# Performance work log

Hardware: AMD Instinct MI355X
Metric: run time of the kernel (lower is better)

The kernel has to match this reference:

```python
import jax, jax.numpy as jnp
import numpy as np

BETA = 0.25


def setup_inputs() -> dict:
    key = jax.random.key(0)
    k1, k2 = jax.random.split(key)
    latents = jax.random.normal(k1, (16, 4096, 256), dtype=jnp.float32)
    K = 1024
    # torch init: uniform(-1/K, 1/K)
    codebook = jax.random.uniform(k2, (K, 256), dtype=jnp.float32, minval=-1.0 / K, maxval=1.0 / K)
    return {"latents": latents, "codebook": codebook}


def reference(latents, codebook):
    D = codebook.shape[1]
    flat = latents.reshape(-1, D)  # [N, D]
    dist = (jnp.sum(flat * flat, axis=1, keepdims=True)
            + jnp.sum(codebook * codebook, axis=1)
            - 2.0 * jnp.matmul(flat, codebook.T))
    encoding_inds = jnp.argmin(dist, axis=1)  # [N]
    # gather nearest codebook vectors (equivalent to one-hot @ codebook)
    quantized = codebook[encoding_inds].reshape(latents.shape)
    commitment_loss = jnp.mean((jax.lax.stop_gradient(quantized) - latents) ** 2)
    embedding_loss = jnp.mean((quantized - jax.lax.stop_gradient(latents)) ** 2)
    vq_loss = commitment_loss * BETA + embedding_loss
    # straight-through estimator
    quantized_st = latents + jax.lax.stop_gradient(quantized - latents)
    return quantized_st, vq_loss
```

## Files before the change

kernel.cpp:

```cpp
#include <hip/hip_runtime.h>

typedef __attribute__((ext_vector_type(4))) float f32x4;
typedef __attribute__((ext_vector_type(2))) long i64x2;

#define SCALE 262144.0f
#define NEG2S -524288.0f
#define INV_S2 1.4551915228366852e-11f

static __device__ __forceinline__ unsigned umin2(unsigned a, unsigned b) { return a < b ? a : b; }

static __device__ __forceinline__ float dec_e4m3(unsigned b) {
  int e = (b >> 3) & 15, m = b & 7;
  float v = e ? ldexpf((float)(8 + m), e - 10) : ldexpf((float)m, -9);
  return (b & 0x80) ? -v : v;
}

__global__ void vq_prep(const float* __restrict__ cb,
                        float* __restrict__ norms,
                        unsigned char* __restrict__ cbh,
                        float* __restrict__ loss_out) {
  if (blockIdx.x == 0 && threadIdx.x == 0) *loss_out = 0.0f;
  const int lane = threadIdx.x & 63;
  const int code = (blockIdx.x * blockDim.x + threadIdx.x) >> 6;
  const f32x4 v = ((const f32x4*)(cb + (long)code * 256))[lane];
  unsigned w = __builtin_amdgcn_cvt_pk_fp8_f32(v[0] * SCALE, v[1] * SCALE, 0, false);
  w = __builtin_amdgcn_cvt_pk_fp8_f32(v[2] * SCALE, v[3] * SCALE, w, true);
  float n = 0.f;
#pragma unroll
  for (int j = 0; j < 4; ++j) {
    float d = dec_e4m3((w >> (8 * j)) & 0xFFu);
    n = __builtin_fmaf(d, d, n);
  }
  const int newpos = ((lane >> 1) & 3) * 64 + (lane >> 3) * 8 + (lane & 1) * 4;
  *(unsigned*)(cbh + (long)code * 256 + newpos) = w;
#pragma unroll
  for (int m = 1; m < 64; m <<= 1) n += __shfl_xor(n, m);
  if (lane == 0) norms[code] = n;
}

#define NTHR 512
#define RPB 256
#define NTILE 16

__global__ __launch_bounds__(NTHR, 2)
void vq_main(const float* __restrict__ X,
             const float* __restrict__ CB,
             const float* __restrict__ norms_g,
             const unsigned char* __restrict__ cbh,
             float* __restrict__ out,
             float* __restrict__ loss_out,
             float lscale) {
  __shared__ __attribute__((aligned(16))) unsigned char Xs[2][4096];
  __shared__ unsigned mgAll[NTILE][8][16];
  __shared__ unsigned idxArr[RPB];
  __shared__ float wsumX[8], wsumS[8];

  const int t = threadIdx.x;
  const int lane = t & 63;
  const int wave = t >> 6;
  const int lo16 = lane & 15;
  const int hi = lane >> 4;
  const long rowBase = (long)blockIdx.x * RPB;

  long b[8][8];
  float nrm[8];
  {
    const char* cbB = (const char*)cbh;
#pragma unroll
    for (int n = 0; n < 8; ++n) {
      const int code = wave * 128 + n * 16 + lo16;
      const char* src = cbB + (long)code * 256 + hi * 64;
#pragma unroll
      for (int kp = 0; kp < 4; ++kp) {
        i64x2 bb = *(const i64x2*)(src + kp * 16);
        b[n][2 * kp] = bb.x;
        b[n][2 * kp + 1] = bb.y;
      }
      nrm[n] = norms_g[code];
    }
  }

  const int srow = t >> 5;
  const int sch = t & 31;
  const unsigned sdst =
      (unsigned)(srow * 256 + ((((sch & 3) * 64) + ((sch >> 2) * 8)) ^ ((srow & 7) << 3)));
  const f32x4* xv = (const f32x4*)(X + (rowBase + srow) * 256) + sch * 2;

  float xn = 0.f;
  f32x4 p0, p1;

#define CVT_WRITE(BUF)                                                                    \
  {                                                                                       \
    float s0 = 0.f;                                                                       \
    _Pragma("unroll") for (int j = 0; j < 4; ++j) s0 = __builtin_fmaf(p0[j], p0[j], s0);  \
    _Pragma("unroll") for (int j = 0; j < 4; ++j) s0 = __builtin_fmaf(p1[j], p1[j], s0);  \
    xn += s0;                                                                             \
    unsigned w0 = __builtin_amdgcn_cvt_pk_fp8_f32(p0[0], p0[1], 0, false);                \
    w0 = __builtin_amdgcn_cvt_pk_fp8_f32(p0[2], p0[3], w0, true);                         \
    unsigned w1 = __builtin_amdgcn_cvt_pk_fp8_f32(p1[0], p1[1], 0, false);                \
    w1 = __builtin_amdgcn_cvt_pk_fp8_f32(p1[2], p1[3], w1, true);                         \
    *(long*)((char*)&Xs[BUF][0] + sdst) = (long)(unsigned)w0 | ((long)w1 << 32);          \
  }

  p0 = __builtin_nontemporal_load(xv);
  p1 = __builtin_nontemporal_load(xv + 1);
  CVT_WRITE(0);
  p0 = __builtin_nontemporal_load(xv + 1024);
  p1 = __builtin_nontemporal_load(xv + 1024 + 1);
  __syncthreads();

  for (int tt = 0; tt < NTILE; ++tt) {
    const char* xb = (const char*)&Xs[tt & 1][0];
    const unsigned abase = (unsigned)(lo16 * 256 + hi * 64);
    const unsigned aswz = (unsigned)((lo16 & 7) << 3);
    long a[8];
#pragma unroll
    for (int ks = 0; ks < 8; ++ks)
      a[ks] = *(const long*)(xb + ((abase + ks * 8) ^ aswz));

    f32x4 acc[8];
#pragma unroll
    for (int n = 0; n < 8; ++n) {
      f32x4 z = {0.f, 0.f, 0.f, 0.f};
      acc[n] = z;
    }
    __builtin_amdgcn_s_setprio(1);
#pragma unroll
    for (int ks = 0; ks < 8; ++ks)
#pragma unroll
      for (int n = 0; n < 8; ++n)
        acc[n] = __builtin_amdgcn_mfma_f32_16x16x32_fp8_fp8(a[ks], b[n][ks], acc[n], 0, 0, 0);
    __builtin_amdgcn_s_setprio(0);

    unsigned bst[4] = {0xFFFFFFFFu, 0xFFFFFFFFu, 0xFFFFFFFFu, 0xFFFFFFFFu};
#pragma unroll
    for (int n = 0; n < 8; ++n) {
      const float nf = nrm[n];
      const unsigned code = (unsigned)(wave * 128 + n * 16 + lo16);
#pragma unroll
      for (int r = 0; r < 4; ++r) {
        float sv = __builtin_fmaf(NEG2S, acc[n][r], nf);
        unsigned u = __float_as_uint(sv);
        u = ((int)u < 0) ? ~u : (u | 0x80000000u);
        bst[r] = umin2(bst[r], (u & 0xFFFFFC00u) | code);
      }
    }
#pragma unroll
    for (int r = 0; r < 4; ++r) {
#pragma unroll
      for (int msk = 1; msk < 16; msk <<= 1)
        bst[r] = umin2(bst[r], (unsigned)__shfl_xor((int)bst[r], msk));
    }
    if (lo16 == 0) {
#pragma unroll
      for (int r = 0; r < 4; ++r) mgAll[tt][wave][hi * 4 + r] = bst[r];
    }

    if (tt + 1 < NTILE) {
      CVT_WRITE((tt + 1) & 1);
      if (tt + 2 < NTILE) {
        p0 = __builtin_nontemporal_load(xv + (tt + 2) * 1024);
        p1 = __builtin_nontemporal_load(xv + (tt + 2) * 1024 + 1);
      }
    }
    __syncthreads();
  }

#pragma unroll
  for (int msk = 1; msk < 64; msk <<= 1) xn += __shfl_xor(xn, msk);
  if (lane == 0) wsumX[wave] = xn;

  float scv = 0.f;
  if (t < RPB) {
    unsigned e = 0xFFFFFFFFu;
#pragma unroll
    for (int w = 0; w < 8; ++w) e = umin2(e, mgAll[t >> 4][w][t & 15]);
    idxArr[t] = e & 1023u;
    unsigned um = (e & 0xFFFFFC00u) | 512u;
    float sr = (um & 0x80000000u) ? __uint_as_float(um & 0x7FFFFFFFu) : __uint_as_float(~um);
    scv = sr * INV_S2;
  }
#pragma unroll
  for (int msk = 1; msk < 64; msk <<= 1) scv += __shfl_xor(scv, msk);
  if (lane == 0) wsumS[wave] = scv;
  __syncthreads();

  {
    const f32x4* CBv = (const f32x4*)CB;
    f32x4* Og = (f32x4*)(out + rowBase * 256);
#pragma unroll 4
    for (int i = 0; i < 32; ++i) {
      int idx = t + NTHR * i;
      int row = idx >> 6, d4 = idx & 63;
      int code = (int)idxArr[row];
      f32x4 e = CBv[code * 64 + d4];
      __builtin_nontemporal_store(e, Og + idx);
    }
  }

  if (t == 0) {
    float tot = 0.f;
#pragma unroll
    for (int w = 0; w < 8; ++w) tot += wsumX[w] + wsumS[w];
    atomicAdd(loss_out, tot * lscale);
  }
}

extern "C" void kernel_launch(void* const* d_in, const int* in_sizes, int n_in,
                              void* d_out, int out_size, void* d_ws, size_t ws_size,
                              hipStream_t stream) {
  const float* X = (const float*)d_in[0];
  const float* CB = (const float*)d_in[1];
  float* out = (float*)d_out;

  const int ND = in_sizes[0];
  const int K = in_sizes[1] / 256;
  const int N = ND / 256;

  float* ws_norms = (float*)d_ws;
  unsigned char* ws_cb = (unsigned char*)((char*)d_ws + 4096);
  float* loss_out = out + (size_t)ND;

  vq_prep<<<K / 4, 256, 0, stream>>>(CB, ws_norms, ws_cb, loss_out);

  const float lscale = 1.25f / (float)ND;
  vq_main<<<N / RPB, NTHR, 0, stream>>>(X, CB, ws_norms, ws_cb, out, loss_out, lscale);
}
```

Before: 62.70 us.

## Split latent FP8 conversion into separate kernel and widen main kernel to 1024 threads

Latent conversion to FP8 and the squared-norm sum move into a new pre-pass kernel. That kernel writes the FP8 rows into the output buffer, which then serves as scratch. The main kernel now uses 1024 threads per block with 64 codes per wave and reads A fragments directly from global memory instead of a double-buffered LDS tile. Per-row argmin uses shared-memory atomicMin in place of a staged merge array, and the gather writes rows per thread group. This removes the LDS staging and the per-tile barriers. The cost is an extra kernel launch, an extra global write and read of the FP8 data, and the output buffer being read while other blocks overwrite it with final values.

```diff
diff --git a/kernel.cpp b/kernel.cpp
--- a/kernel.cpp
+++ b/kernel.cpp
@@ -38,105 +38,95 @@
   if (lane == 0) norms[code] = n;
 }
 
-#define NTHR 512
-#define RPB 256
-#define NTILE 16
+__global__ void vq_xprep(const float* __restrict__ X,
+                         float* __restrict__ out,
+                         float* __restrict__ loss_out,
+                         float lscale) {
+  __shared__ float wsum[4];
+  const int t = threadIdx.x;
+  const long base = (long)blockIdx.x * 1024;
+  float xn = 0.f;
+#pragma unroll
+  for (int i = 0; i < 4; ++i) {
+    long g = base + t + 256 * i;
+    f32x4 v = __builtin_nontemporal_load((const f32x4*)X + g);
+#pragma unroll
+    for (int j = 0; j < 4; ++j) xn = __builtin_fmaf(v[j], v[j], xn);
+    unsigned w = __builtin_amdgcn_cvt_pk_fp8_f32(v[0], v[1], 0, false);
+    w = __builtin_amdgcn_cvt_pk_fp8_f32(v[2], v[3], w, true);
+    long row = g >> 6;
+    int k4 = (int)(g & 63);
+    *(unsigned*)((char*)out + row * 1024 + k4 * 4) = w;
+  }
+#pragma unroll
+  for (int m = 1; m < 64; m <<= 1) xn += __shfl_xor(xn, m);
+  if ((t & 63) == 0) wsum[t >> 6] = xn;
+  __syncthreads();
+  if (t == 0) atomicAdd(loss_out, (wsum[0] + wsum[1] + wsum[2] + wsum[3]) * lscale);
+}
 
-__global__ __launch_bounds__(NTHR, 2)
-void vq_main(const float* __restrict__ X,
-             const float* __restrict__ CB,
+__global__ __launch_bounds__(1024, 4)
+void vq_main(const float* __restrict__ CB,
              const float* __restrict__ norms_g,
              const unsigned char* __restrict__ cbh,
              float* __restrict__ out,
              float* __restrict__ loss_out,
              float lscale) {
-  __shared__ __attribute__((aligned(16))) unsigned char Xs[2][4096];
-  __shared__ unsigned mgAll[NTILE][8][16];
-  __shared__ unsigned idxArr[RPB];
-  __shared__ float wsumX[8], wsumS[8];
+  __shared__ unsigned keys[256];
+  __shared__ float wsum[16];
 
   const int t = threadIdx.x;
   const int lane = t & 63;
   const int wave = t >> 6;
   const int lo16 = lane & 15;
   const int hi = lane >> 4;
-  const long rowBase = (long)blockIdx.x * RPB;
+  const long rowBase = (long)blockIdx.x * 256;
 
-  long b[8][8];
-  float nrm[8];
-  {
-    const char* cbB = (const char*)cbh;
+  if (t < 256) keys[t] = 0xFFFFFFFFu;
+
+  i64x2 b[4][4];
+  float nrm[4];
 #pragma unroll
-    for (int n = 0; n < 8; ++n) {
-      const int code = wave * 128 + n * 16 + lo16;
-      const char* src = cbB + (long)code * 256 + hi * 64;
+  for (int n = 0; n < 4; ++n) {
+    const int code = wave * 64 + n * 16 + lo16;
+    const char* src = (const char*)cbh + (long)code * 256 + hi * 64;
 #pragma unroll
-      for (int kp = 0; kp < 4; ++kp) {
-        i64x2 bb = *(const i64x2*)(src + kp * 16);
-        b[n][2 * kp] = bb.x;
-        b[n][2 * kp + 1] = bb.y;
-      }
-      nrm[n] = norms_g[code];
-    }
+    for (int kp = 0; kp < 4; ++kp) b[n][kp] = *(const i64x2*)(src + kp * 16);
+    nrm[n] = norms_g[code];
   }
-
-  const int srow = t >> 5;
-  const int sch = t & 31;
-  const unsigned sdst =
-      (unsigned)(srow * 256 + ((((sch & 3) * 64) + ((sch >> 2) * 8)) ^ ((srow & 7) << 3)));
-  const f32x4* xv = (const f32x4*)(X + (rowBase + srow) * 256) + sch * 2;
-
-  float xn = 0.f;
-  f32x4 p0, p1;
-
-#define CVT_WRITE(BUF)                                                                    \
-  {                                                                                       \
-    float s0 = 0.f;                                                                       \
-    _Pragma("unroll") for (int j = 0; j < 4; ++j) s0 = __builtin_fmaf(p0[j], p0[j], s0);  \
-    _Pragma("unroll") for (int j = 0; j < 4; ++j) s0 = __builtin_fmaf(p1[j], p1[j], s0);  \
-    xn += s0;                                                                             \
-    unsigned w0 = __builtin_amdgcn_cvt_pk_fp8_f32(p0[0], p0[1], 0, false);                \
-    w0 = __builtin_amdgcn_cvt_pk_fp8_f32(p0[2], p0[3], w0, true);                         \
-    unsigned w1 = __builtin_amdgcn_cvt_pk_fp8_f32(p1[0], p1[1], 0, false);                \
-    w1 = __builtin_amdgcn_cvt_pk_fp8_f32(p1[2], p1[3], w1, true);                         \
-    *(long*)((char*)&Xs[BUF][0] + sdst) = (long)(unsigned)w0 | ((long)w1 << 32);          \
-  }
-
-  p0 = __builtin_nontemporal_load(xv);
-  p1 = __builtin_nontemporal_load(xv + 1);
-  CVT_WRITE(0);
-  p0 = __builtin_nontemporal_load(xv + 1024);
-  p1 = __builtin_nontemporal_load(xv + 1024 + 1);
   __syncthreads();
 
-  for (int tt = 0; tt < NTILE; ++tt) {
-    const char* xb = (const char*)&Xs[tt & 1][0];
-    const unsigned abase = (unsigned)(lo16 * 256 + hi * 64);
-    const unsigned aswz = (unsigned)((lo16 & 7) << 3);
+  const char* x8 = (const char*)out;
+  const unsigned laneOff = (unsigned)(lo16 * 1024 + hi * 8);
+
+  for (int tile = 0; tile < 16; ++tile) {
+    const char* xb = x8 + (rowBase + tile * 16) * 1024 + laneOff;
     long a[8];
 #pragma unroll
-    for (int ks = 0; ks < 8; ++ks)
-      a[ks] = *(const long*)(xb + ((abase + ks * 8) ^ aswz));
+    for (int ks = 0; ks < 8; ++ks) a[ks] = *(const long*)(xb + ks * 32);
 
-    f32x4 acc[8];
+    f32x4 acc[4];
 #pragma unroll
-    for (int n = 0; n < 8; ++n) {
+    for (int n = 0; n < 4; ++n) {
       f32x4 z = {0.f, 0.f, 0.f, 0.f};
       acc[n] = z;
     }
     __builtin_amdgcn_s_setprio(1);
 #pragma unroll
-    for (int ks = 0; ks < 8; ++ks)
+    for (int kp = 0; kp < 4; ++kp) {
 #pragma unroll
-      for (int n = 0; n < 8; ++n)
-        acc[n] = __builtin_amdgcn_mfma_f32_16x16x32_fp8_fp8(a[ks], b[n][ks], acc[n], 0, 0, 0);
+      for (int n = 0; n < 4; ++n) {
+        acc[n] = __builtin_amdgcn_mfma_f32_16x16x32_fp8_fp8(a[2 * kp], b[n][kp].x, acc[n], 0, 0, 0);
+        acc[n] = __builtin_amdgcn_mfma_f32_16x16x32_fp8_fp8(a[2 * kp + 1], b[n][kp].y, acc[n], 0, 0, 0);
+      }
+    }
     __builtin_amdgcn_s_setprio(0);
 
     unsigned bst[4] = {0xFFFFFFFFu, 0xFFFFFFFFu, 0xFFFFFFFFu, 0xFFFFFFFFu};
 #pragma unroll
-    for (int n = 0; n < 8; ++n) {
+    for (int n = 0; n < 4; ++n) {
       const float nf = nrm[n];
-      const unsigned code = (unsigned)(wave * 128 + n * 16 + lo16);
+      const unsigned code = (unsigned)(wave * 64 + n * 16 + lo16);
 #pragma unroll
       for (int r = 0; r < 4; ++r) {
         float sv = __builtin_fmaf(NEG2S, acc[n][r], nf);
@@ -151,57 +141,35 @@
       for (int msk = 1; msk < 16; msk <<= 1)
         bst[r] = umin2(bst[r], (unsigned)__shfl_xor((int)bst[r], msk));
     }
-    if (lo16 == 0) {
-#pragma unroll
-      for (int r = 0; r < 4; ++r) mgAll[tt][wave][hi * 4 + r] = bst[r];
-    }
-
-    if (tt + 1 < NTILE) {
-      CVT_WRITE((tt + 1) & 1);
-      if (tt + 2 < NTILE) {
-        p0 = __builtin_nontemporal_load(xv + (tt + 2) * 1024);
-        p1 = __builtin_nontemporal_load(xv + (tt + 2) * 1024 + 1);
-      }
-    }
-    __syncthreads();
+    if (lo16 < 4) atomicMin(&keys[tile * 16 + hi * 4 + lo16], bst[lo16]);
   }
 
+  __syncthreads();
+
+  float sc = 0.f;
+  {
+    const int row = t >> 2;
+    const int q = t & 3;
+    const unsigned e = keys[row];
+    const int code = (int)(e & 1023u);
+    if (q == 0) {
+      unsigned um = (e & 0xFFFFFC00u) | 512u;
+      float sr = (um & 0x80000000u) ? __uint_as_float(um & 0x7FFFFFFFu) : __uint_as_float(~um);
+      sc = sr * INV_S2;
+    }
+    const f32x4* src = (const f32x4*)CB + code * 64 + q;
+    f32x4* dst = (f32x4*)out + (rowBase + row) * 64 + q;
 #pragma unroll
-  for (int msk = 1; msk < 64; msk <<= 1) xn += __shfl_xor(xn, msk);
-  if (lane == 0) wsumX[wave] = xn;
-
-  float scv = 0.f;
-  if (t < RPB) {
-    unsigned e = 0xFFFFFFFFu;
-#pragma unroll
-    for (int w = 0; w < 8; ++w) e = umin2(e, mgAll[t >> 4][w][t & 15]);
-    idxArr[t] = e & 1023u;
-    unsigned um = (e & 0xFFFFFC00u) | 512u;
-    float sr = (um & 0x80000000u) ? __uint_as_float(um & 0x7FFFFFFFu) : __uint_as_float(~um);
-    scv = sr * INV_S2;
+    for (int j = 0; j < 16; ++j) __builtin_nontemporal_store(src[4 * j], dst + 4 * j);
   }
 #pragma unroll
-  for (int msk = 1; msk < 64; msk <<= 1) scv += __shfl_xor(scv, msk);
-  if (lane == 0) wsumS[wave] = scv;
+  for (int m = 1; m < 64; m <<= 1) sc += __shfl_xor(sc, m);
+  if (lane == 0) wsum[wave] = sc;
   __syncthreads();
-
-  {
-    const f32x4* CBv = (const f32x4*)CB;
-    f32x4* Og = (f32x4*)(out + rowBase * 256);
-#pragma unroll 4
-    for (int i = 0; i < 32; ++i) {
-      int idx = t + NTHR * i;
-      int row = idx >> 6, d4 = idx & 63;
-      int code = (int)idxArr[row];
-      f32x4 e = CBv[code * 64 + d4];
-      __builtin_nontemporal_store(e, Og + idx);
-    }
-  }
-
   if (t == 0) {
     float tot = 0.f;
 #pragma unroll
-    for (int w = 0; w < 8; ++w) tot += wsumX[w] + wsumS[w];
+    for (int w = 0; w < 16; ++w) tot += wsum[w];
     atomicAdd(loss_out, tot * lscale);
   }
 }
@@ -221,8 +189,9 @@
   unsigned char* ws_cb = (unsigned char*)((char*)d_ws + 4096);
   float* loss_out = out + (size_t)ND;
 
+  const float lscale = 1.25f / (float)ND;
+
   vq_prep<<<K / 4, 256, 0, stream>>>(CB, ws_norms, ws_cb, loss_out);
-
-  const float lscale = 1.25f / (float)ND;
-  vq_main<<<N / RPB, NTHR, 0, stream>>>(X, CB, ws_norms, ws_cb, out, loss_out, lscale);
+  vq_xprep<<<ND / 4096, 256, 0, stream>>>(X, out, loss_out, lscale);
+  vq_main<<<N / 256, 1024, 0, stream>>>(CB, ws_norms, ws_cb, out, loss_out, lscale);
 }
```

Result: slower. 162.9 us (+159.8%).
